# Performance work log

Measured on AMD Instinct MI355X. Metric: run time of the kernel, lower is better.

The kernel has to match this reference:

```python
import jax, jax.numpy as jnp
import numpy as np

B, N, E, F = 4, 4096, 65536, 128


def setup_inputs() -> dict:
    key = jax.random.key(0)
    ks = jax.random.split(key, 16)
    s = 0.02
    inp = {
        'node_feats': jax.random.normal(ks[0], (B, N, F), jnp.float32),
        'edge_feats': jax.random.normal(ks[1], (B, E, F), jnp.float32),
        'i': jax.random.randint(ks[2], (E,), 0, N, jnp.int32),
        'j': jax.random.randint(ks[3], (E,), 0, N, jnp.int32),
        'W_src_gate': jax.random.normal(ks[4], (F, F), jnp.float32) * s,
        'b_src_gate': jnp.zeros((F,), jnp.float32),
        'W_dst_gate': jax.random.normal(ks[5], (F, F), jnp.float32) * s,
        'b_dst_gate': jnp.zeros((F,), jnp.float32),
        'W_edge_gate': jax.random.normal(ks[6], (F, F), jnp.float32) * s,
        'b_edge_gate': jnp.zeros((F,), jnp.float32),
        'W_src_update': jax.random.normal(ks[7], (F, F), jnp.float32) * s,
        'b_src_update': jnp.zeros((F,), jnp.float32),
        'W_dst_update': jax.random.normal(ks[8], (F, F), jnp.float32) * s,
        'b_dst_update': jnp.zeros((F,), jnp.float32),
    }
    return inp


def _linear(x, W, b):
    # torch nn.Linear: x @ W.T + b, W is [out, in]
    return jnp.einsum('bnf,gf->bng', x, W) + b


def reference(node_feats, edge_feats, i, j,
              W_src_gate, b_src_gate, W_dst_gate, b_dst_gate,
              W_edge_gate, b_edge_gate, W_src_update, b_src_update,
              W_dst_update, b_dst_update):
    Bn, Nn, Fn = node_feats.shape
    e_src = _linear(node_feats, W_src_gate, b_src_gate)[:, i]      # [B, E, F]
    e_dst = _linear(node_feats, W_dst_gate, b_dst_gate)[:, j]      # [B, E, F]
    y = e_src + e_dst + _linear(edge_feats, W_edge_gate, b_edge_gate)
    sigma = jax.nn.sigmoid(y)
    bh = _linear(node_feats, W_dst_update, b_dst_update)[:, j]     # [B, E, F]
    m = bh * sigma
    # scatter-add over edges into destination nodes (along dim 1)
    zeros = jnp.zeros((Bn, Nn, Fn), node_feats.dtype)
    sum_sigma_h = zeros.at[:, i].add(m)
    sum_sigma = zeros.at[:, i].add(sigma)
    h = sum_sigma_h / (sum_sigma + 1e-6)
    x = jax.nn.silu(_linear(node_feats, W_src_update, b_src_update) + h)
    y = jax.nn.silu(y)
    # residual=True
    x = node_feats + x
    y = edge_feats + y
    return (x, y)
```

## Files before the change

### kernel.cpp

```cpp
#include <hip/hip_runtime.h>
#include <hip/hip_bf16.h>

typedef __attribute__((ext_vector_type(8))) short short8;
typedef __attribute__((ext_vector_type(4))) float f32x4;
typedef __attribute__((ext_vector_type(2))) float f32x2;

#define DEVI __device__ __forceinline__

static constexpr int NB = 4;
static constexpr int NN = 4096;
static constexpr int NE = 65536;
static constexpr int MROWS = NB * NN;

DEVI short f2b(float f) {
    __hip_bfloat16 h = __float2bfloat16(f);
    return *reinterpret_cast<short*>(&h);
}
DEVI float b2f(ushort u) {
    uint v = (uint)u << 16;
    float f;
    __builtin_memcpy(&f, &v, 4);
    return f;
}

__global__ void prep_weights(const float* __restrict__ w0, const float* __restrict__ w1,
                             const float* __restrict__ w2, const float* __restrict__ w3,
                             const float* __restrict__ w4, ushort* __restrict__ out) {
    int idx = blockIdx.x * 256 + threadIdx.x;
    int wsel = idx >> 14;
    int off = idx & 16383;
    const float* src = wsel == 0 ? w0 : wsel == 1 ? w1 : wsel == 2 ? w2 : wsel == 3 ? w3 : w4;
    out[idx] = (ushort)f2b(src[off]);
}

__global__ void hist_kernel(const int* __restrict__ iIdx, int* __restrict__ cnt) {
    int e = blockIdx.x * 256 + threadIdx.x;
    atomicAdd(&cnt[iIdx[e]], 1);
}

__global__ __launch_bounds__(256) void scan_kernel(const int* __restrict__ cnt,
                                                   int* __restrict__ start) {
    __shared__ int ls[256];
    int t = threadIdx.x;
    int base = t * 16;
    int loc[16];
    int s = 0;
#pragma unroll
    for (int q = 0; q < 16; ++q) { loc[q] = s; s += cnt[base + q]; }
    ls[t] = s;
    __syncthreads();
    for (int off = 1; off < 256; off <<= 1) {
        int v = (t >= off) ? ls[t - off] : 0;
        __syncthreads();
        ls[t] += v;
        __syncthreads();
    }
    int ex = ls[t] - s;
#pragma unroll
    for (int q = 0; q < 16; ++q) start[base + q] = ex + loc[q];
    if (t == 255) start[4096] = ex + s;
}

__global__ void scatter_kernel(const int* __restrict__ iIdx, const int* __restrict__ jIdx,
                               const int* __restrict__ start, int* __restrict__ cur,
                               int* __restrict__ rank, int* __restrict__ jsort) {
    int e = blockIdx.x * 256 + threadIdx.x;
    int iv = iIdx[e];
    int pos = start[iv] + atomicAdd(&cur[iv], 1);
    rank[e] = pos;
    jsort[pos] = jIdx[e];
}

DEVI void stage_W256(const ushort* __restrict__ Wg, ushort* Wl, int tid) {
    int n = tid >> 1;
    int kh = (tid & 1) * 64;
#pragma unroll
    for (int c = 0; c < 8; ++c) {
        int k = kh + c * 8;
        short8 v = *reinterpret_cast<const short8*>(Wg + n * 128 + k);
        int byt = (n * 256 + k * 2) ^ ((n & 7) << 4);
        *reinterpret_cast<short8*>(reinterpret_cast<char*>(Wl) + byt) = v;
    }
}

DEVI void stage_W512(const ushort* __restrict__ Wg, ushort* Wl, int tid) {
    int n = tid >> 2;
    int kq = (tid & 3) * 32;
#pragma unroll
    for (int c = 0; c < 4; ++c) {
        int k = kq + c * 8;
        short8 v = *reinterpret_cast<const short8*>(Wg + n * 128 + k);
        int byt = (n * 256 + k * 2) ^ ((n & 7) << 4);
        *reinterpret_cast<short8*>(reinterpret_cast<char*>(Wl) + byt) = v;
    }
}

DEVI void load_afrag(const float* __restrict__ rowptr, int kgrp, short8 afrag[4]) {
#pragma unroll
    for (int ks = 0; ks < 4; ++ks) {
        int k0 = ks * 32 + kgrp * 8;
        f32x4 lo = *reinterpret_cast<const f32x4*>(rowptr + k0);
        f32x4 hi = *reinterpret_cast<const f32x4*>(rowptr + k0 + 4);
        short8 a;
#pragma unroll
        for (int q = 0; q < 4; ++q) a[q] = f2b(lo[q]);
#pragma unroll
        for (int q = 0; q < 4; ++q) a[4 + q] = f2b(hi[q]);
        afrag[ks] = a;
    }
}

DEVI void mfma_frags(const short8 afrag[4], const ushort* __restrict__ Wl,
                     int lane, f32x4 acc[8]) {
    const int colb = lane & 15;
    const int kgrp = lane >> 4;
#pragma unroll
    for (int nt = 0; nt < 8; ++nt) acc[nt] = f32x4{0.f, 0.f, 0.f, 0.f};
#pragma unroll
    for (int ks = 0; ks < 4; ++ks) {
#pragma unroll
        for (int nt = 0; nt < 8; ++nt) {
            int n = nt * 16 + colb;
            int byt = (n * 256 + (ks * 32 + kgrp * 8) * 2) ^ ((n & 7) << 4);
            short8 bfrag = *reinterpret_cast<const short8*>(
                reinterpret_cast<const char*>(Wl) + byt);
            acc[nt] = __builtin_amdgcn_mfma_f32_16x16x32_bf16(afrag[ks], bfrag, acc[nt], 0, 0, 0);
        }
    }
}

__global__ __launch_bounds__(256) void node_proj_kernel(
    const float* __restrict__ node_feats,
    const ushort* __restrict__ Wbf,
    const float* __restrict__ bias0, const float* __restrict__ bias1,
    const float* __restrict__ bias2, const float* __restrict__ bias3,
    ushort* __restrict__ P)
{
    __shared__ ushort Wl[128 * 128];
    const int widx = blockIdx.y;
    const int row0 = blockIdx.x * 64;
    const int tid = threadIdx.x;

    stage_W256(Wbf + (size_t)widx * 16384, Wl, tid);
    __syncthreads();

    const int lane = tid & 63, wv = tid >> 6;
    const int colb = lane & 15, kgrp = lane >> 4;
    short8 afrag[4];
    load_afrag(node_feats + (size_t)(row0 + wv * 16 + colb) * 128, kgrp, afrag);
    f32x4 acc[8];
    mfma_frags(afrag, Wl, lane, acc);

    const float* bias = widx == 0 ? bias0 : widx == 1 ? bias1 : widx == 2 ? bias2 : bias3;
    ushort* Po = P + (size_t)widx * MROWS * 128;
#pragma unroll
    for (int r = 0; r < 4; ++r) {
        int row = row0 + wv * 16 + kgrp * 4 + r;
#pragma unroll
        for (int nt = 0; nt < 8; ++nt) {
            int col = nt * 16 + colb;
            Po[(size_t)row * 128 + col] = (ushort)f2b(acc[nt][r] + bias[col]);
        }
    }
}

__global__ __launch_bounds__(512, 4) void edge_kernel(
    const float* __restrict__ edge_feats,
    const int* __restrict__ iIdx, const int* __restrict__ jIdx,
    const int* __restrict__ rank,
    const ushort* __restrict__ Weg,
    const float* __restrict__ b_eg,
    const ushort* __restrict__ Psg, const ushort* __restrict__ Pdg,
    ushort* __restrict__ sigS,
    float* __restrict__ yOut)
{
    __shared__ ushort Wl[128 * 128];
    const int b = blockIdx.y;
    const int e0 = blockIdx.x * 128;
    const int tid = threadIdx.x;

    stage_W512(Weg, Wl, tid);
    __syncthreads();

    const int lane = tid & 63, wv = tid >> 6;
    const int colb = lane & 15, kgrp = lane >> 4;
    const float* Ab = edge_feats + (size_t)b * NE * 128;
    const size_t nbase = (size_t)b * NN;

    short8 afrag[4];
    load_afrag(Ab + (size_t)(e0 + wv * 16 + colb) * 128, kgrp, afrag);
    f32x4 acc[8];
    mfma_frags(afrag, Wl, lane, acc);

#pragma unroll
    for (int r = 0; r < 4; ++r) {
        int erow = wv * 16 + kgrp * 4 + r;
        int e = e0 + erow;
        int ie = iIdx[e], je = jIdx[e], rk = rank[e];
        const ushort* sg = Psg + (nbase + ie) * 128;
        const ushort* dg = Pdg + (nbase + je) * 128;
        const float* ef = Ab + (size_t)(e0 + erow) * 128;
        float* yo = yOut + ((size_t)b * NE + e) * 128;
        ushort* so = sigS + ((size_t)b * NE + rk) * 128;
#pragma unroll
        for (int nt = 0; nt < 8; ++nt) {
            int col = nt * 16 + colb;
            float y = acc[nt][r] + b_eg[col] + b2f(sg[col]) + b2f(dg[col]);
            float sig = 1.0f / (1.0f + __expf(-y));
            yo[col] = ef[col] + y * sig;
            so[col] = (ushort)f2b(sig);
        }
    }
}

__global__ __launch_bounds__(256, 8) void node_reduce_kernel(
    const ushort* __restrict__ sigS,
    const int* __restrict__ start,
    const int* __restrict__ jsort,
    const ushort* __restrict__ Pdu,
    const ushort* __restrict__ Psu,
    const float* __restrict__ nf,
    float* __restrict__ xOut)
{
    int task = blockIdx.x * 4 + (threadIdx.x >> 6);
    int lane = threadIdx.x & 63;
    int b = task >> 12;
    int n = task & 4095;
    int s0 = start[n], s1 = start[n + 1];

    const size_t ebase = (size_t)b * NE;
    const size_t nbase = (size_t)b * NN;

    float S0 = 0.f, S1 = 0.f, Sh0 = 0.f, Sh1 = 0.f;
    int k = s0;
    for (; k + 4 <= s1; k += 4) {
        uint sv[4], dv[4];
#pragma unroll
        for (int q = 0; q < 4; ++q) {
            int j = jsort[k + q];
            sv[q] = *reinterpret_cast<const uint*>(sigS + (ebase + k + q) * 128 + lane * 2);
            dv[q] = *reinterpret_cast<const uint*>(Pdu + (nbase + j) * 128 + lane * 2);
        }
#pragma unroll
        for (int q = 0; q < 4; ++q) {
            float sa = b2f((ushort)(sv[q] & 0xffff)), sb = b2f((ushort)(sv[q] >> 16));
            float da = b2f((ushort)(dv[q] & 0xffff)), db = b2f((ushort)(dv[q] >> 16));
            S0 += sa; S1 += sb;
            Sh0 += da * sa; Sh1 += db * sb;
        }
    }
    for (; k < s1; ++k) {
        int j = jsort[k];
        uint sg2 = *reinterpret_cast<const uint*>(sigS + (ebase + k) * 128 + lane * 2);
        uint du2 = *reinterpret_cast<const uint*>(Pdu + (nbase + j) * 128 + lane * 2);
        float sa = b2f((ushort)(sg2 & 0xffff)), sb = b2f((ushort)(sg2 >> 16));
        float da = b2f((ushort)(du2 & 0xffff)), db = b2f((ushort)(du2 >> 16));
        S0 += sa; S1 += sb;
        Sh0 += da * sa; Sh1 += db * sb;
    }

    size_t off = (nbase + n) * 128 + lane * 2;
    uint su2 = *reinterpret_cast<const uint*>(Psu + off);
    f32x2 a = *reinterpret_cast<const f32x2*>(nf + off);
    float h0 = Sh0 / (S0 + 1e-6f);
    float h1 = Sh1 / (S1 + 1e-6f);
    float v0 = b2f((ushort)(su2 & 0xffff)) + h0;
    float v1 = b2f((ushort)(su2 >> 16)) + h1;
    f32x2 r;
    r[0] = a[0] + v0 / (1.f + __expf(-v0));
    r[1] = a[1] + v1 / (1.f + __expf(-v1));
    *reinterpret_cast<f32x2*>(xOut + off) = r;
}

extern "C" void kernel_launch(void* const* d_in, const int* in_sizes, int n_in,
                              void* d_out, int out_size, void* d_ws, size_t ws_size,
                              hipStream_t stream) {
    (void)in_sizes; (void)n_in; (void)out_size; (void)ws_size;

    const float* node_feats = (const float*)d_in[0];
    const float* edge_feats = (const float*)d_in[1];
    const int* iIdx = (const int*)d_in[2];
    const int* jIdx = (const int*)d_in[3];
    const float* Wsg = (const float*)d_in[4];  const float* bsg = (const float*)d_in[5];
    const float* Wdg = (const float*)d_in[6];  const float* bdg = (const float*)d_in[7];
    const float* Weg = (const float*)d_in[8];  const float* beg = (const float*)d_in[9];
    const float* Wsu = (const float*)d_in[10]; const float* bsu = (const float*)d_in[11];
    const float* Wdu = (const float*)d_in[12]; const float* bdu = (const float*)d_in[13];

    float* out = (float*)d_out;
    float* xOut = out;
    float* yOut = out + (size_t)MROWS * 128;

    ushort* sigS = (ushort*)d_ws;
    ushort* P = sigS + (size_t)NB * NE * 128;
    ushort* Wbf = P + (size_t)4 * MROWS * 128;
    int* rank = (int*)(Wbf + 5 * 16384);
    int* jsort = rank + NE;
    int* cnt = jsort + NE;
    int* cur = cnt + 4096;
    int* start = cur + 4096;

    hipMemsetAsync(cnt, 0, 2 * 4096 * sizeof(int), stream);

    prep_weights<<<(5 * 16384) / 256, 256, 0, stream>>>(Wsg, Wdg, Wdu, Wsu, Weg, Wbf);

    hist_kernel<<<NE / 256, 256, 0, stream>>>(iIdx, cnt);
    scan_kernel<<<1, 256, 0, stream>>>(cnt, start);
    scatter_kernel<<<NE / 256, 256, 0, stream>>>(iIdx, jIdx, start, cur, rank, jsort);

    dim3 gA(MROWS / 64, 4);
    node_proj_kernel<<<gA, 256, 0, stream>>>(node_feats, Wbf, bsg, bdg, bdu, bsu, P);

    dim3 gB(NE / 128, NB);
    edge_kernel<<<gB, 512, 0, stream>>>(edge_feats, iIdx, jIdx, rank,
                                        Wbf + (size_t)4 * 16384, beg,
                                        P,
                                        P + (size_t)1 * MROWS * 128,
                                        sigS, yOut);

    node_reduce_kernel<<<MROWS / 4, 256, 0, stream>>>(
        sigS, start, jsort,
        P + (size_t)2 * MROWS * 128,
        P + (size_t)3 * MROWS * 128,
        node_feats, xOut);
}
```

Before: 161.4 us.

## Fuse segment reduction into edge kernel with sorted-order atomics

The edge kernel now walks edges in destination-sorted order through a permutation. It accumulates sigma and sigma*Pdu per run of equal i in registers and flushes the partial sums with float atomics into node-level S/Sh buffers. This removes the bf16 sigma round-trip through global memory and the separate per-node gather-reduce kernel, which a light finalize kernel replaces. In exchange, edge_feats reads and y writes become row-permuted (non-contiguous), a 16 MB memset is added, and atomics make the summation order nondeterministic.

```diff
diff --git a/kernel.cpp b/kernel.cpp
--- a/kernel.cpp
+++ b/kernel.cpp
@@ -63,11 +63,13 @@
 
 __global__ void scatter_kernel(const int* __restrict__ iIdx, const int* __restrict__ jIdx,
                                const int* __restrict__ start, int* __restrict__ cur,
-                               int* __restrict__ rank, int* __restrict__ jsort) {
+                               int* __restrict__ perm, int* __restrict__ isort,
+                               int* __restrict__ jsort) {
     int e = blockIdx.x * 256 + threadIdx.x;
     int iv = iIdx[e];
     int pos = start[iv] + atomicAdd(&cur[iv], 1);
-    rank[e] = pos;
+    perm[pos] = e;
+    isort[pos] = iv;
     jsort[pos] = jIdx[e];
 }
 
@@ -166,19 +168,27 @@
 
 __global__ __launch_bounds__(512, 4) void edge_kernel(
     const float* __restrict__ edge_feats,
-    const int* __restrict__ iIdx, const int* __restrict__ jIdx,
-    const int* __restrict__ rank,
+    const int* __restrict__ perm,
+    const int* __restrict__ isort,
+    const int* __restrict__ jsort,
     const ushort* __restrict__ Weg,
     const float* __restrict__ b_eg,
     const ushort* __restrict__ Psg, const ushort* __restrict__ Pdg,
-    ushort* __restrict__ sigS,
+    const ushort* __restrict__ Pdu,
+    float* __restrict__ Sh, float* __restrict__ S,
     float* __restrict__ yOut)
 {
     __shared__ ushort Wl[128 * 128];
+    __shared__ int eL[128], iL[128], jL[128];
     const int b = blockIdx.y;
-    const int e0 = blockIdx.x * 128;
+    const int k0 = blockIdx.x * 128;
     const int tid = threadIdx.x;
 
+    if (tid < 128) {
+        eL[tid] = perm[k0 + tid];
+        iL[tid] = isort[k0 + tid];
+        jL[tid] = jsort[k0 + tid];
+    }
     stage_W512(Weg, Wl, tid);
     __syncthreads();
 
@@ -188,84 +198,69 @@
     const size_t nbase = (size_t)b * NN;
 
     short8 afrag[4];
-    load_afrag(Ab + (size_t)(e0 + wv * 16 + colb) * 128, kgrp, afrag);
+    load_afrag(Ab + (size_t)eL[wv * 16 + colb] * 128, kgrp, afrag);
     f32x4 acc[8];
     mfma_frags(afrag, Wl, lane, acc);
 
+    float Sacc[8], Shacc[8];
+#pragma unroll
+    for (int nt = 0; nt < 8; ++nt) { Sacc[nt] = 0.f; Shacc[nt] = 0.f; }
+    int previ = iL[wv * 16 + kgrp * 4];
+
 #pragma unroll
     for (int r = 0; r < 4; ++r) {
-        int erow = wv * 16 + kgrp * 4 + r;
-        int e = e0 + erow;
-        int ie = iIdx[e], je = jIdx[e], rk = rank[e];
+        int srow = wv * 16 + kgrp * 4 + r;
+        int e = eL[srow], ie = iL[srow], je = jL[srow];
+        if (ie != previ) {
+            size_t o = (nbase + previ) * 128;
+#pragma unroll
+            for (int nt = 0; nt < 8; ++nt) {
+                int col = nt * 16 + colb;
+                atomicAdd(&S[o + col], Sacc[nt]);
+                atomicAdd(&Sh[o + col], Shacc[nt]);
+                Sacc[nt] = 0.f; Shacc[nt] = 0.f;
+            }
+            previ = ie;
+        }
         const ushort* sg = Psg + (nbase + ie) * 128;
         const ushort* dg = Pdg + (nbase + je) * 128;
-        const float* ef = Ab + (size_t)(e0 + erow) * 128;
+        const ushort* du = Pdu + (nbase + je) * 128;
+        const float* ef = Ab + (size_t)e * 128;
         float* yo = yOut + ((size_t)b * NE + e) * 128;
-        ushort* so = sigS + ((size_t)b * NE + rk) * 128;
 #pragma unroll
         for (int nt = 0; nt < 8; ++nt) {
             int col = nt * 16 + colb;
             float y = acc[nt][r] + b_eg[col] + b2f(sg[col]) + b2f(dg[col]);
             float sig = 1.0f / (1.0f + __expf(-y));
             yo[col] = ef[col] + y * sig;
-            so[col] = (ushort)f2b(sig);
-        }
-    }
-}
-
-__global__ __launch_bounds__(256, 8) void node_reduce_kernel(
-    const ushort* __restrict__ sigS,
-    const int* __restrict__ start,
-    const int* __restrict__ jsort,
-    const ushort* __restrict__ Pdu,
-    const ushort* __restrict__ Psu,
-    const float* __restrict__ nf,
+            Sacc[nt] += sig;
+            Shacc[nt] += b2f(du[col]) * sig;
+        }
+    }
+    {
+        size_t o = (nbase + previ) * 128;
+#pragma unroll
+        for (int nt = 0; nt < 8; ++nt) {
+            int col = nt * 16 + colb;
+            atomicAdd(&S[o + col], Sacc[nt]);
+            atomicAdd(&Sh[o + col], Shacc[nt]);
+        }
+    }
+}
+
+__global__ __launch_bounds__(256) void finalize_kernel(
+    const float* __restrict__ nf, const ushort* __restrict__ Psu,
+    const float* __restrict__ Sh, const float* __restrict__ S,
     float* __restrict__ xOut)
 {
-    int task = blockIdx.x * 4 + (threadIdx.x >> 6);
-    int lane = threadIdx.x & 63;
-    int b = task >> 12;
-    int n = task & 4095;
-    int s0 = start[n], s1 = start[n + 1];
-
-    const size_t ebase = (size_t)b * NE;
-    const size_t nbase = (size_t)b * NN;
-
-    float S0 = 0.f, S1 = 0.f, Sh0 = 0.f, Sh1 = 0.f;
-    int k = s0;
-    for (; k + 4 <= s1; k += 4) {
-        uint sv[4], dv[4];
-#pragma unroll
-        for (int q = 0; q < 4; ++q) {
-            int j = jsort[k + q];
-            sv[q] = *reinterpret_cast<const uint*>(sigS + (ebase + k + q) * 128 + lane * 2);
-            dv[q] = *reinterpret_cast<const uint*>(Pdu + (nbase + j) * 128 + lane * 2);
-        }
-#pragma unroll
-        for (int q = 0; q < 4; ++q) {
-            float sa = b2f((ushort)(sv[q] & 0xffff)), sb = b2f((ushort)(sv[q] >> 16));
-            float da = b2f((ushort)(dv[q] & 0xffff)), db = b2f((ushort)(dv[q] >> 16));
-            S0 += sa; S1 += sb;
-            Sh0 += da * sa; Sh1 += db * sb;
-        }
-    }
-    for (; k < s1; ++k) {
-        int j = jsort[k];
-        uint sg2 = *reinterpret_cast<const uint*>(sigS + (ebase + k) * 128 + lane * 2);
-        uint du2 = *reinterpret_cast<const uint*>(Pdu + (nbase + j) * 128 + lane * 2);
-        float sa = b2f((ushort)(sg2 & 0xffff)), sb = b2f((ushort)(sg2 >> 16));
-        float da = b2f((ushort)(du2 & 0xffff)), db = b2f((ushort)(du2 >> 16));
-        S0 += sa; S1 += sb;
-        Sh0 += da * sa; Sh1 += db * sb;
-    }
-
-    size_t off = (nbase + n) * 128 + lane * 2;
+    int idx = blockIdx.x * 256 + threadIdx.x;
+    size_t off = (size_t)idx * 2;
     uint su2 = *reinterpret_cast<const uint*>(Psu + off);
     f32x2 a = *reinterpret_cast<const f32x2*>(nf + off);
-    float h0 = Sh0 / (S0 + 1e-6f);
-    float h1 = Sh1 / (S1 + 1e-6f);
-    float v0 = b2f((ushort)(su2 & 0xffff)) + h0;
-    float v1 = b2f((ushort)(su2 >> 16)) + h1;
+    f32x2 sh = *reinterpret_cast<const f32x2*>(Sh + off);
+    f32x2 s = *reinterpret_cast<const f32x2*>(S + off);
+    float v0 = b2f((ushort)(su2 & 0xffff)) + sh[0] / (s[0] + 1e-6f);
+    float v1 = b2f((ushort)(su2 >> 16)) + sh[1] / (s[1] + 1e-6f);
     f32x2 r;
     r[0] = a[0] + v0 / (1.f + __expf(-v0));
     r[1] = a[1] + v1 / (1.f + __expf(-v1));
@@ -291,36 +286,37 @@
     float* xOut = out;
     float* yOut = out + (size_t)MROWS * 128;
 
-    ushort* sigS = (ushort*)d_ws;
-    ushort* P = sigS + (size_t)NB * NE * 128;
+    float* Sh = (float*)d_ws;
+    float* S = Sh + (size_t)MROWS * 128;
+    ushort* P = (ushort*)(S + (size_t)MROWS * 128);
     ushort* Wbf = P + (size_t)4 * MROWS * 128;
-    int* rank = (int*)(Wbf + 5 * 16384);
-    int* jsort = rank + NE;
+    int* perm = (int*)(Wbf + 5 * 16384);
+    int* isort = perm + NE;
+    int* jsort = isort + NE;
     int* cnt = jsort + NE;
     int* cur = cnt + 4096;
     int* start = cur + 4096;
 
+    hipMemsetAsync(Sh, 0, (size_t)2 * MROWS * 128 * sizeof(float), stream);
     hipMemsetAsync(cnt, 0, 2 * 4096 * sizeof(int), stream);
 
     prep_weights<<<(5 * 16384) / 256, 256, 0, stream>>>(Wsg, Wdg, Wdu, Wsu, Weg, Wbf);
 
     hist_kernel<<<NE / 256, 256, 0, stream>>>(iIdx, cnt);
     scan_kernel<<<1, 256, 0, stream>>>(cnt, start);
-    scatter_kernel<<<NE / 256, 256, 0, stream>>>(iIdx, jIdx, start, cur, rank, jsort);
+    scatter_kernel<<<NE / 256, 256, 0, stream>>>(iIdx, jIdx, start, cur, perm, isort, jsort);
 
     dim3 gA(MROWS / 64, 4);
     node_proj_kernel<<<gA, 256, 0, stream>>>(node_feats, Wbf, bsg, bdg, bdu, bsu, P);
 
     dim3 gB(NE / 128, NB);
-    edge_kernel<<<gB, 512, 0, stream>>>(edge_feats, iIdx, jIdx, rank,
+    edge_kernel<<<gB, 512, 0, stream>>>(edge_feats, perm, isort, jsort,
                                         Wbf + (size_t)4 * 16384, beg,
                                         P,
                                         P + (size_t)1 * MROWS * 128,
-                                        sigS, yOut);
-
-    node_reduce_kernel<<<MROWS / 4, 256, 0, stream>>>(
-        sigS, start, jsort,
-        P + (size_t)2 * MROWS * 128,
-        P + (size_t)3 * MROWS * 128,
-        node_feats, xOut);
-}
+                                        P + (size_t)2 * MROWS * 128,
+                                        Sh, S, yOut);
+
+    finalize_kernel<<<(MROWS * 64) / 256, 256, 0, stream>>>(
+        node_feats, P + (size_t)3 * MROWS * 128, Sh, S, xOut);
+}
```

Measured after the change: 275.3 us. +70.6%, slower.
